# Kernel optimization log

Hardware: AMD Instinct MI355X
Metric: run time of the kernel (lower is better)

Reference implementation:

```python
import jax, jax.numpy as jnp
import numpy as np

B_, NWIN, WH, WW = 8, 256, 8, 8
DIM, HEADS = 192, 6
N = WH * WW


def setup_inputs() -> dict:
    key = jax.random.key(0)
    ks = jax.random.split(key, 5)
    return {
        "x": jax.random.normal(ks[0], (B_, NWIN, N, DIM), dtype=jnp.float32),
        "qkv_w": jax.random.normal(ks[1], (3 * DIM, DIM), dtype=jnp.float32) * 0.02,
        "qkv_b": jax.random.normal(ks[2], (3 * DIM,), dtype=jnp.float32) * 0.02,
        "proj_w": jax.random.normal(ks[3], (DIM, DIM), dtype=jnp.float32) * 0.02,
        "proj_b": jax.random.normal(ks[4], (DIM,), dtype=jnp.float32) * 0.02,
    }


def _grad_magnitude(t, B, H, n, d, Wh, Ww):
    # t: [B,H,n,N,d] -> spatial layout [B,H,n,d,Wh,Ww]
    t = jnp.swapaxes(t, 3, 4).reshape(B, H, n, d, Wh, Ww)
    # forward finite difference with zero pre-pad (matches conv2d [-1,1] pad=1 then slice)
    gx = t - jnp.concatenate([jnp.zeros_like(t[..., :1]), t[..., :-1]], axis=-1)
    gy = t - jnp.concatenate([jnp.zeros_like(t[..., :1, :]), t[..., :-1, :]], axis=-2)
    return jnp.sum(jnp.abs(gx) + jnp.abs(gy), axis=(-1, -2))  # [B,H,n,d]


def reference(x, qkv_w, qkv_b, proj_w, proj_b):
    B, n, Ntok, C = x.shape
    H = HEADS
    d = C // H
    scale = d ** (-0.5)
    qkv = x @ qkv_w.T + qkv_b                       # [B,n,N,3C]
    qkv = qkv.reshape(B, n, Ntok, 3, H, d)
    qkv = jnp.transpose(qkv, (3, 0, 4, 1, 2, 5))    # [3,B,H,n,N,d]
    q, k, v = qkv[0] * scale, qkv[1], qkv[2]
    qg = _grad_magnitude(q, B, H, n, d, WH, WW)     # [B,H,n,d]
    kg = _grad_magnitude(k, B, H, n, d, WH, WW)
    qg = jnp.swapaxes(qg, 2, 3)[..., None]          # [B,H,d,n,1]
    kg = jnp.swapaxes(kg, 2, 3)[..., None]          # [B,H,d,n,1]
    attn = qg @ jnp.swapaxes(kg, -1, -2)            # [B,H,d,n,n] rank-1 scores
    attn = jax.nn.softmax(attn, axis=-1)
    vp = jnp.transpose(v, (0, 1, 4, 2, 3))          # [B,H,d,n,N]
    out = attn @ vp                                 # [B,H,d,n,N]
    out = jnp.transpose(out, (0, 3, 4, 1, 2)).reshape(B * n, Ntok, C)
    return out @ proj_w.T + proj_b                  # [B*n, N, C]
```

## Files before the change

### kernel.cpp

```cpp
#include <hip/hip_runtime.h>
#include <cstddef>


#define SCALE 0.17677669529663687f

typedef __attribute__((ext_vector_type(8))) short short8;
typedef __attribute__((ext_vector_type(4))) float f32x4;

__device__ __forceinline__ unsigned short f2bf(float f) {
    unsigned u = __float_as_uint(f);
    u += 0x7fffu + ((u >> 16) & 1u);
    return (unsigned short)(u >> 16);
}
__device__ __forceinline__ float bf2f(unsigned int h) {
    return __uint_as_float(h << 16);
}
__device__ __forceinline__ unsigned pack2(unsigned short a, unsigned short b) {
    return (unsigned)a | ((unsigned)b << 16);
}

__global__ __launch_bounds__(256) void wsplit_kernel(
    const float* __restrict__ w, unsigned short* __restrict__ Wh,
    unsigned short* __restrict__ Wl)
{
    int idx = blockIdx.x * 256 + threadIdx.x;
    float v = w[idx];
    unsigned short h = f2bf(v);
    Wh[idx] = h;
    if (idx < 73728) Wl[idx] = f2bf(v - bf2f(h));
}

__global__ __launch_bounds__(256) void wproj_kernel(
    const float* __restrict__ w, unsigned short* __restrict__ Wp)
{
    int idx = blockIdx.x * 256 + threadIdx.x;
    Wp[idx] = f2bf(w[idx]);
}

__global__ __launch_bounds__(512, 2) void qkv_fused_kernel(
    const float* __restrict__ x, const unsigned short* __restrict__ Wh,
    const unsigned short* __restrict__ Wl, const float* __restrict__ bias,
    unsigned short* __restrict__ vT, float* __restrict__ qg, float* __restrict__ kg)
{
    __shared__ unsigned short As_h[128 * 40];
    __shared__ unsigned short As_l[128 * 40];
    __shared__ unsigned short Bs_h[576 * 40];
    __shared__ unsigned short Bs_l[384 * 40];

    const int tid = threadIdx.x;
    const int wave = tid >> 6, lane = tid & 63;
    const int quad = lane >> 4, col = lane & 15;
    const int wq = wave & 3, wofs = (wave >> 2) * 64;
    const int m0 = blockIdx.x * 128;

    const int arow = tid >> 2;
    const int apart = (tid & 3) * 8;
    const float* xp = x + (size_t)(m0 + arow) * 192 + apart;

    f32x4 acc[9][4];
#pragma unroll
    for (int s = 0; s < 9; ++s)
#pragma unroll
        for (int mi = 0; mi < 4; ++mi) {
            f32x4 z = {0.f, 0.f, 0.f, 0.f};
            acc[s][mi] = z;
        }

    float4 pa0, pa1;
    uint4 pbh[5], pbl[3];

    auto load_chunk = [&](int kk) {
        const int k0 = kk * 32;
        pa0 = *(const float4*)(xp + k0);
        pa1 = *(const float4*)(xp + k0 + 4);
#pragma unroll
        for (int i = 0; i < 5; ++i) {
            int idx = tid + i * 512;
            if (idx < 2304)
                pbh[i] = *(const uint4*)(Wh + (size_t)(idx >> 2) * 192 + k0 + (idx & 3) * 8);
        }
#pragma unroll
        for (int i = 0; i < 3; ++i) {
            int idx = tid + i * 512;
            pbl[i] = *(const uint4*)(Wl + (size_t)(idx >> 2) * 192 + k0 + (idx & 3) * 8);
        }
    };

    auto write_chunk = [&]() {
        float v[8] = {pa0.x, pa0.y, pa0.z, pa0.w, pa1.x, pa1.y, pa1.z, pa1.w};
        unsigned short h[8], l[8];
#pragma unroll
        for (int i = 0; i < 8; ++i) {
            h[i] = f2bf(v[i]);
            l[i] = f2bf(v[i] - bf2f(h[i]));
        }
        uint4 H = make_uint4(pack2(h[0], h[1]), pack2(h[2], h[3]),
                             pack2(h[4], h[5]), pack2(h[6], h[7]));
        uint4 L = make_uint4(pack2(l[0], l[1]), pack2(l[2], l[3]),
                             pack2(l[4], l[5]), pack2(l[6], l[7]));
        *(uint4*)&As_h[arow * 40 + apart] = H;
        *(uint4*)&As_l[arow * 40 + apart] = L;
#pragma unroll
        for (int i = 0; i < 5; ++i) {
            int idx = tid + i * 512;
            if (idx < 2304)
                *(uint4*)&Bs_h[(idx >> 2) * 40 + (idx & 3) * 8] = pbh[i];
        }
#pragma unroll
        for (int i = 0; i < 3; ++i) {
            int idx = tid + i * 512;
            *(uint4*)&Bs_l[(idx >> 2) * 40 + (idx & 3) * 8] = pbl[i];
        }
    };

    load_chunk(0);
    for (int kk = 0; kk < 6; ++kk) {
        __syncthreads();
        write_chunk();
        __syncthreads();
        if (kk < 5) load_chunk(kk + 1);

        short8 ah[4], al[4];
#pragma unroll
        for (int mi = 0; mi < 4; ++mi) {
            int r = wofs + mi * 16 + col;
            ah[mi] = *(const short8*)&As_h[r * 40 + quad * 8];
            al[mi] = *(const short8*)&As_l[r * 40 + quad * 8];
        }
#pragma unroll
        for (int s = 0; s < 9; ++s) {
            const int nr = (wq + s * 4) * 16 + col;
            short8 bh = *(const short8*)&Bs_h[nr * 40 + quad * 8];
            if (s < 6) {
                short8 bl = *(const short8*)&Bs_l[nr * 40 + quad * 8];
#pragma unroll
                for (int mi = 0; mi < 4; ++mi) {
                    acc[s][mi] = __builtin_amdgcn_mfma_f32_16x16x32_bf16(al[mi], bh, acc[s][mi], 0, 0, 0);
                    acc[s][mi] = __builtin_amdgcn_mfma_f32_16x16x32_bf16(ah[mi], bl, acc[s][mi], 0, 0, 0);
                    acc[s][mi] = __builtin_amdgcn_mfma_f32_16x16x32_bf16(ah[mi], bh, acc[s][mi], 0, 0, 0);
                }
            } else {
#pragma unroll
                for (int mi = 0; mi < 4; ++mi)
                    acc[s][mi] = __builtin_amdgcn_mfma_f32_16x16x32_bf16(ah[mi], bh, acc[s][mi], 0, 0, 0);
            }
        }
    }

#pragma unroll
    for (int s = 0; s < 9; ++s) {
        float bv = bias[(wq + s * 4) * 16 + col];
#pragma unroll
        for (int mi = 0; mi < 4; ++mi)
#pragma unroll
            for (int r = 0; r < 4; ++r)
                acc[s][mi][r] += bv;
    }

    const int gw = blockIdx.x * 2 + (wave >> 2);
    const int b = gw >> 8, win = gw & 255;

#pragma unroll
    for (int s = 0; s < 6; ++s) {
        const int n = wq + s * 4;
        float yx[4][4], p3[4];
#pragma unroll
        for (int mi = 0; mi < 4; ++mi) {
#pragma unroll
            for (int r = 0; r < 4; ++r)
                yx[mi][r] = __shfl_xor(acc[s][mi][r], 32);
            p3[mi] = __shfl_xor(acc[s][mi][3], 16);
        }
        float sum = 0.f;
#pragma unroll
        for (int mi = 0; mi < 4; ++mi)
#pragma unroll
            for (int r = 0; r < 4; ++r) {
                float v = acc[s][mi][r];
                float gx = (r > 0) ? (v - acc[s][mi][r - 1])
                                   : ((quad & 1) ? (v - p3[mi]) : v);
                float gy = (quad >= 2) ? (v - yx[mi][r])
                                       : ((mi > 0) ? (v - yx[mi - 1][r]) : v);
                sum += fabsf(gx) + fabsf(gy);
            }
        sum += __shfl_xor(sum, 16);
        sum += __shfl_xor(sum, 32);
        float* dst = (s < 3) ? qg : kg;
        const int chb = ((s < 3) ? n : n - 12) * 16;
        const float sc = (s < 3) ? SCALE : 1.0f;
        if (lane < 16)
            dst[(size_t)(b * 192 + chb + lane) * 256 + win] = sum * sc;
    }
#pragma unroll
    for (int s = 6; s < 9; ++s) {
        const int ch = (wq + s * 4 - 24) * 16 + col;
#pragma unroll
        for (int mi = 0; mi < 4; ++mi) {
            int tok0 = mi * 16 + quad * 4;
            ushort4 o = make_ushort4(f2bf(acc[s][mi][0]), f2bf(acc[s][mi][1]),
                                     f2bf(acc[s][mi][2]), f2bf(acc[s][mi][3]));
            *(ushort4*)(vT + (size_t)(b * 192 + ch) * 16384 + win * 64 + tok0) = o;
        }
    }
}

__global__ __launch_bounds__(256) void attn_mfma_kernel(
    const unsigned short* __restrict__ vT, const float* __restrict__ qg,
    const float* __restrict__ kg, unsigned short* __restrict__ attbuf)
{
    __shared__ unsigned short Vs[64 * 264];
    __shared__ float kds[256];
    __shared__ float red[256];

    const int g = blockIdx.x;
    const int tid = threadIdx.x;
    const int wave = tid >> 6, lane = tid & 63;
    const int quad = lane >> 4, col = lane & 15;

    float kv = kg[(size_t)g * 256 + tid];
    red[tid] = kv;
    __syncthreads();
    for (int s = 128; s > 0; s >>= 1) {
        if (tid < s) red[tid] = fmaxf(red[tid], red[tid + s]);
        __syncthreads();
    }
    kds[tid] = kv - red[0];

    const unsigned short* vb = vT + (size_t)g * 16384;
    {
        const int jr = tid >> 3;
        const int tb = (tid & 7) * 8;
#pragma unroll
        for (int it = 0; it < 8; ++it) {
            int j = it * 32 + jr;
            uint4 u = *(const uint4*)(vb + (size_t)j * 64 + tb);
            Vs[(tb + 0) * 264 + j] = (unsigned short)(u.x & 0xffffu);
            Vs[(tb + 1) * 264 + j] = (unsigned short)(u.x >> 16);
            Vs[(tb + 2) * 264 + j] = (unsigned short)(u.y & 0xffffu);
            Vs[(tb + 3) * 264 + j] = (unsigned short)(u.y >> 16);
            Vs[(tb + 4) * 264 + j] = (unsigned short)(u.z & 0xffffu);
            Vs[(tb + 5) * 264 + j] = (unsigned short)(u.z >> 16);
            Vs[(tb + 6) * 264 + j] = (unsigned short)(u.w & 0xffffu);
            Vs[(tb + 7) * 264 + j] = (unsigned short)(u.w >> 16);
        }
    }

    float ai[4];
#pragma unroll
    for (int mi = 0; mi < 4; ++mi)
        ai[mi] = qg[(size_t)g * 256 + wave * 64 + mi * 16 + col];

    __syncthreads();

    f32x4 acc[4][4];
#pragma unroll
    for (int mi = 0; mi < 4; ++mi)
#pragma unroll
        for (int ni = 0; ni < 4; ++ni) {
            f32x4 z = {0.f, 0.f, 0.f, 0.f};
            acc[mi][ni] = z;
        }
    float den[4] = {0.f, 0.f, 0.f, 0.f};

    for (int kt = 0; kt < 8; ++kt) {
        const int k0 = kt * 32;
        float4 ka = *(const float4*)&kds[k0 + quad * 8];
        float4 kb = *(const float4*)&kds[k0 + quad * 8 + 4];
        float kv8[8] = {ka.x, ka.y, ka.z, ka.w, kb.x, kb.y, kb.z, kb.w};

        short8 bfr[4];
#pragma unroll
        for (int ni = 0; ni < 4; ++ni)
            bfr[ni] = *(const short8*)&Vs[(ni * 16 + col) * 264 + k0 + quad * 8];

#pragma unroll
        for (int mi = 0; mi < 4; ++mi) {
            short8 ef;
            float dl = 0.f;
#pragma unroll
            for (int j = 0; j < 8; ++j) {
                float e = __expf(ai[mi] * kv8[j]);
                unsigned short h = f2bf(e);
                ef[j] = (short)h;
                dl += bf2f(h);
            }
            den[mi] += dl;
#pragma unroll
            for (int ni = 0; ni < 4; ++ni)
                acc[mi][ni] = __builtin_amdgcn_mfma_f32_16x16x32_bf16(
                    ef, bfr[ni], acc[mi][ni], 0, 0, 0);
        }
    }

#pragma unroll
    for (int mi = 0; mi < 4; ++mi) {
        den[mi] += __shfl_xor(den[mi], 16);
        den[mi] += __shfl_xor(den[mi], 32);
    }

    unsigned short* ob = attbuf + (size_t)g * 16384;
#pragma unroll
    for (int mi = 0; mi < 4; ++mi) {
        float invr[4];
#pragma unroll
        for (int r = 0; r < 4; ++r)
            invr[r] = 1.0f / __shfl(den[mi], quad * 4 + r);
#pragma unroll
        for (int ni = 0; ni < 4; ++ni)
#pragma unroll
            for (int r = 0; r < 4; ++r) {
                int i = wave * 64 + mi * 16 + quad * 4 + r;
                int tok = ni * 16 + col;
                ob[i * 64 + tok] = f2bf(acc[mi][ni][r] * invr[r]);
            }
    }
}

__global__ __launch_bounds__(256) void proj_mfma_kernel(
    const unsigned short* __restrict__ attbuf, const unsigned short* __restrict__ Wp,
    const float* __restrict__ bias, float* __restrict__ out)
{
    __shared__ unsigned short Bs[64 * 40];
    __shared__ float T[32 * 197];

    const int tid = threadIdx.x;
    const int wave = tid >> 6, lane = tid & 63;
    const int quad = lane >> 4, col = lane & 15;
    const int rowg0 = blockIdx.x * 64;
    const int b = rowg0 >> 14;
    const int rl0 = rowg0 & 16383;
    const unsigned short* ab = attbuf + (size_t)b * 3145728;

    f32x4 acc[3][4];
#pragma unroll
    for (int mi = 0; mi < 3; ++mi)
#pragma unroll
        for (int ni = 0; ni < 4; ++ni) {
            f32x4 z = {0.f, 0.f, 0.f, 0.f};
            acc[mi][ni] = z;
        }

    const int chl = tid >> 3;
    const int rb = (tid & 7) * 8;

    for (int kt = 0; kt < 6; ++kt) {
        __syncthreads();
        {
            uint4 u = *(const uint4*)(ab + (size_t)(kt * 32 + chl) * 16384 + rl0 + rb);
            Bs[(rb + 0) * 40 + chl] = (unsigned short)(u.x & 0xffffu);
            Bs[(rb + 1) * 40 + chl] = (unsigned short)(u.x >> 16);
            Bs[(rb + 2) * 40 + chl] = (unsigned short)(u.y & 0xffffu);
            Bs[(rb + 3) * 40 + chl] = (unsigned short)(u.y >> 16);
            Bs[(rb + 4) * 40 + chl] = (unsigned short)(u.z & 0xffffu);
            Bs[(rb + 5) * 40 + chl] = (unsigned short)(u.z >> 16);
            Bs[(rb + 6) * 40 + chl] = (unsigned short)(u.w & 0xffffu);
            Bs[(rb + 7) * 40 + chl] = (unsigned short)(u.w >> 16);
        }
        __syncthreads();

        short8 bfr[4], af[3];
#pragma unroll
        for (int ni = 0; ni < 4; ++ni)
            bfr[ni] = *(const short8*)&Bs[(ni * 16 + col) * 40 + quad * 8];
#pragma unroll
        for (int mi = 0; mi < 3; ++mi)
            af[mi] = *(const short8*)(Wp + (size_t)(wave * 48 + mi * 16 + col) * 192
                                      + kt * 32 + quad * 8);
#pragma unroll
        for (int mi = 0; mi < 3; ++mi)
#pragma unroll
            for (int ni = 0; ni < 4; ++ni)
                acc[mi][ni] = __builtin_amdgcn_mfma_f32_16x16x32_bf16(
                    af[mi], bfr[ni], acc[mi][ni], 0, 0, 0);
    }

    float br[3][4];
#pragma unroll
    for (int mi = 0; mi < 3; ++mi)
#pragma unroll
        for (int r = 0; r < 4; ++r)
            br[mi][r] = bias[wave * 48 + mi * 16 + quad * 4 + r];

#pragma unroll
    for (int h = 0; h < 2; ++h) {
        __syncthreads();
#pragma unroll
        for (int nh = 0; nh < 2; ++nh) {
            int ni = h * 2 + nh;
#pragma unroll
            for (int mi = 0; mi < 3; ++mi)
#pragma unroll
                for (int r = 0; r < 4; ++r)
                    T[(nh * 16 + col) * 197 + wave * 48 + mi * 16 + quad * 4 + r] =
                        acc[mi][ni][r] + br[mi][r];
        }
        __syncthreads();
        {
            int row = tid >> 3;
            int ck = (tid & 7) * 24;
            float* op = out + (size_t)(rowg0 + h * 32 + row) * 192 + ck;
#pragma unroll
            for (int q4 = 0; q4 < 6; ++q4) {
                float4 o = make_float4(T[row * 197 + ck + q4 * 4 + 0],
                                       T[row * 197 + ck + q4 * 4 + 1],
                                       T[row * 197 + ck + q4 * 4 + 2],
                                       T[row * 197 + ck + q4 * 4 + 3]);
                *(float4*)(op + q4 * 4) = o;
            }
        }
    }
}

extern "C" void kernel_launch(void* const* d_in, const int* in_sizes, int n_in,
                              void* d_out, int out_size, void* d_ws, size_t ws_size,
                              hipStream_t stream) {
    const float* x      = (const float*)d_in[0];
    const float* qkv_w  = (const float*)d_in[1];
    const float* qkv_b  = (const float*)d_in[2];
    const float* proj_w = (const float*)d_in[3];
    const float* proj_b = (const float*)d_in[4];
    float* out = (float*)d_out;

    unsigned short* base16 = (unsigned short*)d_ws;
    unsigned short* vT16   = base16;
    unsigned short* attbuf = base16 + 25165824;
    float* qg = (float*)(base16 + 50331648);
    float* kg = qg + 393216;
    unsigned short* Wh = (unsigned short*)(kg + 393216);
    unsigned short* Wl = Wh + 110592;
    unsigned short* Wp = Wl + 73728;

    wsplit_kernel<<<432, 256, 0, stream>>>(qkv_w, Wh, Wl);
    wproj_kernel<<<144, 256, 0, stream>>>(proj_w, Wp);
    qkv_fused_kernel<<<1024, 512, 0, stream>>>(x, Wh, Wl, qkv_b, vT16, qg, kg);
    attn_mfma_kernel<<<1536, 256, 0, stream>>>(vT16, qg, kg, attbuf);
    proj_mfma_kernel<<<2048, 256, 0, stream>>>(attbuf, Wp, proj_b, out);
}
```

Measured before the change: 364.2 us.

## Load QKV weights directly into registers and double-buffer A tiles in LDS

Weight fragments are no longer staged through shared memory. Each wave reads its B operand (hi and lo bf16 splits) straight from global/L2 into registers in MFMA fragment layout. The A tile now uses a double-buffered, fragment-ordered LDS layout, which drops one of the two barriers per k-step. This cuts LDS footprint and shared-memory traffic and may raise occupancy. In exchange, global weight loads are duplicated across waves and blocks and depend on cache hits, and register pressure grows.

```diff
diff --git a/kernel.cpp b/kernel.cpp
--- a/kernel.cpp
+++ b/kernel.cpp
@@ -42,20 +42,23 @@
     const unsigned short* __restrict__ Wl, const float* __restrict__ bias,
     unsigned short* __restrict__ vT, float* __restrict__ qg, float* __restrict__ kg)
 {
-    __shared__ unsigned short As_h[128 * 40];
-    __shared__ unsigned short As_l[128 * 40];
-    __shared__ unsigned short Bs_h[576 * 40];
-    __shared__ unsigned short Bs_l[384 * 40];
+    __shared__ unsigned short As_h[2 * 128 * 32];
+    __shared__ unsigned short As_l[2 * 128 * 32];
 
     const int tid = threadIdx.x;
     const int wave = tid >> 6, lane = tid & 63;
     const int quad = lane >> 4, col = lane & 15;
-    const int wq = wave & 3, wofs = (wave >> 2) * 64;
+    const int wq = wave & 3;
+    const int wofs4 = (wave >> 2) * 4;
     const int m0 = blockIdx.x * 128;
 
     const int arow = tid >> 2;
-    const int apart = (tid & 3) * 8;
-    const float* xp = x + (size_t)(m0 + arow) * 192 + apart;
+    const int apart = tid & 3;
+    const float* xp = x + (size_t)(m0 + arow) * 192 + apart * 8;
+    const int aslot = (((arow >> 4) * 64) + apart * 16 + (arow & 15)) * 8;
+
+    const unsigned short* wh_base = Wh + (size_t)(wq * 16 + col) * 192 + quad * 8;
+    const unsigned short* wl_base = Wl + (size_t)(wq * 16 + col) * 192 + quad * 8;
 
     f32x4 acc[9][4];
 #pragma unroll
@@ -67,26 +70,11 @@
         }
 
     float4 pa0, pa1;
-    uint4 pbh[5], pbl[3];
-
     auto load_chunk = [&](int kk) {
-        const int k0 = kk * 32;
-        pa0 = *(const float4*)(xp + k0);
-        pa1 = *(const float4*)(xp + k0 + 4);
-#pragma unroll
-        for (int i = 0; i < 5; ++i) {
-            int idx = tid + i * 512;
-            if (idx < 2304)
-                pbh[i] = *(const uint4*)(Wh + (size_t)(idx >> 2) * 192 + k0 + (idx & 3) * 8);
-        }
-#pragma unroll
-        for (int i = 0; i < 3; ++i) {
-            int idx = tid + i * 512;
-            pbl[i] = *(const uint4*)(Wl + (size_t)(idx >> 2) * 192 + k0 + (idx & 3) * 8);
-        }
+        pa0 = *(const float4*)(xp + kk * 32);
+        pa1 = *(const float4*)(xp + kk * 32 + 4);
     };
-
-    auto write_chunk = [&]() {
+    auto write_chunk = [&](int nb) {
         float v[8] = {pa0.x, pa0.y, pa0.z, pa0.w, pa1.x, pa1.y, pa1.z, pa1.w};
         unsigned short h[8], l[8];
 #pragma unroll
@@ -98,41 +86,44 @@
                              pack2(h[4], h[5]), pack2(h[6], h[7]));
         uint4 L = make_uint4(pack2(l[0], l[1]), pack2(l[2], l[3]),
                              pack2(l[4], l[5]), pack2(l[6], l[7]));
-        *(uint4*)&As_h[arow * 40 + apart] = H;
-        *(uint4*)&As_l[arow * 40 + apart] = L;
-#pragma unroll
-        for (int i = 0; i < 5; ++i) {
-            int idx = tid + i * 512;
-            if (idx < 2304)
-                *(uint4*)&Bs_h[(idx >> 2) * 40 + (idx & 3) * 8] = pbh[i];
-        }
-#pragma unroll
-        for (int i = 0; i < 3; ++i) {
-            int idx = tid + i * 512;
-            *(uint4*)&Bs_l[(idx >> 2) * 40 + (idx & 3) * 8] = pbl[i];
-        }
+        *(uint4*)&As_h[nb * 4096 + aslot] = H;
+        *(uint4*)&As_l[nb * 4096 + aslot] = L;
     };
 
+    int ro8[4];
+#pragma unroll
+    for (int mi = 0; mi < 4; ++mi)
+        ro8[mi] = ((wofs4 + mi) * 64 + quad * 16 + col) * 8;
+
     load_chunk(0);
+    write_chunk(0);
+    __syncthreads();
+
     for (int kk = 0; kk < 6; ++kk) {
-        __syncthreads();
-        write_chunk();
-        __syncthreads();
+        const int cur = kk & 1;
         if (kk < 5) load_chunk(kk + 1);
 
+        const int kw = kk * 32;
+        uint4 pbh[9], pbl[6];
+#pragma unroll
+        for (int s = 0; s < 9; ++s)
+            pbh[s] = *(const uint4*)(wh_base + s * 12288 + kw);
+#pragma unroll
+        for (int s = 0; s < 6; ++s)
+            pbl[s] = *(const uint4*)(wl_base + s * 12288 + kw);
+
         short8 ah[4], al[4];
 #pragma unroll
         for (int mi = 0; mi < 4; ++mi) {
-            int r = wofs + mi * 16 + col;
-            ah[mi] = *(const short8*)&As_h[r * 40 + quad * 8];
-            al[mi] = *(const short8*)&As_l[r * 40 + quad * 8];
-        }
+            ah[mi] = *(const short8*)&As_h[cur * 4096 + ro8[mi]];
+            al[mi] = *(const short8*)&As_l[cur * 4096 + ro8[mi]];
+        }
+
 #pragma unroll
         for (int s = 0; s < 9; ++s) {
-            const int nr = (wq + s * 4) * 16 + col;
-            short8 bh = *(const short8*)&Bs_h[nr * 40 + quad * 8];
+            short8 bh = *(const short8*)&pbh[s];
             if (s < 6) {
-                short8 bl = *(const short8*)&Bs_l[nr * 40 + quad * 8];
+                short8 bl = *(const short8*)&pbl[s];
 #pragma unroll
                 for (int mi = 0; mi < 4; ++mi) {
                     acc[s][mi] = __builtin_amdgcn_mfma_f32_16x16x32_bf16(al[mi], bh, acc[s][mi], 0, 0, 0);
@@ -145,6 +136,9 @@
                     acc[s][mi] = __builtin_amdgcn_mfma_f32_16x16x32_bf16(ah[mi], bh, acc[s][mi], 0, 0, 0);
             }
         }
+
+        if (kk < 5) write_chunk(1 - cur);
+        __syncthreads();
     }
 
 #pragma unroll
```

Result: no change. 370.5 us (+1.7%).
